# Kernel tuning notes

Hardware: AMD Instinct MI355X
Metric: run time of the kernel (lower is better)

Reference implementation:

```python
import jax, jax.numpy as jnp
import numpy as np

B, N, D_MODEL, H, DK, DV = 2, 2048, 512, 8, 64, 64


def setup_inputs() -> dict:
    key = jax.random.key(0)
    ks = jax.random.split(key, 15)
    s = 0.02
    f = jnp.float32
    inp = {
        "x": jax.random.normal(ks[0], (B, N, D_MODEL), f),
        # frozen base projections
        "Wq": jax.random.normal(ks[1], (D_MODEL, H * DK), f) * s,
        "bq": jax.random.normal(ks[2], (H * DK,), f) * s,
        "Wk": jax.random.normal(ks[3], (D_MODEL, H * DK), f) * s,
        "bk": jax.random.normal(ks[4], (H * DK,), f) * s,
        "Wv": jax.random.normal(ks[5], (D_MODEL, H * DV), f) * s,
        "bv": jax.random.normal(ks[6], (H * DV,), f) * s,
        # 'lora' adapters (full linears in the source, added to base)
        "Wq_lora": jax.random.normal(ks[7], (D_MODEL, H * DK), f) * s,
        "bq_lora": jax.random.normal(ks[8], (H * DK,), f) * s,
        "Wk_lora": jax.random.normal(ks[9], (D_MODEL, H * DK), f) * s,
        "bk_lora": jax.random.normal(ks[10], (H * DK,), f) * s,
        "Wv_lora": jax.random.normal(ks[11], (D_MODEL, H * DV), f) * s,
        "bv_lora": jax.random.normal(ks[12], (H * DV,), f) * s,
        # output projection
        "Wo": jax.random.normal(ks[13], (H * DV, D_MODEL), f) * s,
        "bo": jax.random.normal(ks[14], (D_MODEL,), f) * s,
    }
    return inp


def reference(x, Wq, bq, Wk, bk, Wv, bv,
              Wq_lora, bq_lora, Wk_lora, bk_lora, Wv_lora, bv_lora,
              Wo, bo):
    b, n, _ = x.shape
    # base + lora pairs share the same input -> fuse into single GEMMs
    q = x @ (Wq + Wq_lora) + (bq + bq_lora)          # [b, n, H*DK]
    k = x @ (Wk + Wk_lora) + (bk + bk_lora)          # [b, n, H*DK]
    v = x @ (Wv + Wv_lora) + (bv + bv_lora)          # [b, n, H*DV]

    q = q.reshape(b, n, H, DK).transpose(0, 2, 1, 3)  # [b, H, n, DK]
    k = k.reshape(b, n, H, DK).transpose(0, 2, 1, 3)
    v = v.reshape(b, n, H, DV).transpose(0, 2, 1, 3)

    scale = 1.0 / jnp.sqrt(jnp.asarray(DK, x.dtype))
    scores = jnp.einsum('bhqd,bhkd->bhqk', q, k) * scale  # [b, H, n, n]
    att = jax.nn.softmax(scores, axis=-1)                 # attn dropout = eval identity
    out = jnp.einsum('bhqk,bhkd->bhqd', att, v)           # [b, H, n, DV]
    out = out.transpose(0, 2, 1, 3).reshape(b, n, H * DV)
    return out @ Wo + bo                                  # resid dropout = eval identity
```

## Files before the change

kernel.cpp:

```cpp
#include <hip/hip_runtime.h>
#include <hip/hip_bf16.h>

#define B_  2
#define N_  2048
#define DM_ 512
#define H_  8
#define DK_ 64
#define DV_ 64
#define BN_ (B_*N_)
#define SPLITS 2

typedef __attribute__((ext_vector_type(8))) short short8;
typedef __attribute__((ext_vector_type(4))) float f32x4;
typedef unsigned short ushort;
typedef __attribute__((address_space(3))) unsigned int lds_u32_t;
typedef const __attribute__((address_space(1))) unsigned int glb_u32_t;

static __device__ __forceinline__ ushort f2bf(float x) {
    unsigned int u = __float_as_uint(x);
    unsigned int r = (u + 0x7FFFu + ((u >> 16) & 1u)) >> 16;
    return (ushort)r;
}
static __device__ __forceinline__ float bf2f(ushort u) {
    return __uint_as_float(((unsigned)u) << 16);
}
static __device__ __forceinline__ float exp2_fast(float x) {
    float r; asm("v_exp_f32 %0, %1" : "=v"(r) : "v"(x)); return r;
}
static __device__ __forceinline__ unsigned cvt_pk_bf16(float a, float b) {
    unsigned r; asm("v_cvt_pk_bf16_f32 %0, %1, %2" : "=v"(r) : "v"(a), "v"(b)); return r;
}

#define LOG2E 1.4426950408889634f

__global__ __launch_bounds__(256) void fuse_transpose4(
        const float* __restrict__ W0, const float* __restrict__ L0,
        const float* __restrict__ W1, const float* __restrict__ L1,
        const float* __restrict__ W2, const float* __restrict__ L2,
        const float* __restrict__ W3, ushort* __restrict__ WtBase) {
    const int z = blockIdx.z;
    const float* W  = (z == 0) ? W0 : (z == 1) ? W1 : (z == 2) ? W2 : W3;
    const float* WL = (z == 0) ? L0 : (z == 1) ? L1 : (z == 2) ? L2 : nullptr;
    ushort* Wt = WtBase + (size_t)z * DM_ * DM_;

    __shared__ float Ws[32][65];
    const int t  = threadIdx.x;
    const int c0 = blockIdx.x * 64;
    const int k0 = blockIdx.y * 32;
    {
        int r = t >> 4, cq = t & 15;
#pragma unroll
        for (int it = 0; it < 2; ++it) {
            int rr = r + it * 16;
            float4 v = *reinterpret_cast<const float4*>(W + (size_t)(k0 + rr) * DM_ + c0 + cq * 4);
            if (WL) {
                float4 u = *reinterpret_cast<const float4*>(WL + (size_t)(k0 + rr) * DM_ + c0 + cq * 4);
                v.x += u.x; v.y += u.y; v.z += u.z; v.w += u.w;
            }
            Ws[rr][cq * 4 + 0] = v.x; Ws[rr][cq * 4 + 1] = v.y;
            Ws[rr][cq * 4 + 2] = v.z; Ws[rr][cq * 4 + 3] = v.w;
        }
    }
    __syncthreads();
    {
        int cr = t >> 2, kq = t & 3;
        short8 o;
#pragma unroll
        for (int j = 0; j < 8; ++j) o[j] = (short)f2bf(Ws[kq * 8 + j][cr]);
        *reinterpret_cast<short8*>(Wt + (size_t)(c0 + cr) * DM_ + k0 + kq * 8) = o;
    }
}

__global__ void xcast_bias(const float* __restrict__ x, ushort* __restrict__ xb,
                           const float* __restrict__ bq, const float* __restrict__ bqL,
                           const float* __restrict__ bk, const float* __restrict__ bkL,
                           const float* __restrict__ bv, const float* __restrict__ bvL,
                           float* __restrict__ fb) {
    const int bid = blockIdx.x;
    if (bid < 1024) {
        size_t idx = (size_t)bid * blockDim.x + threadIdx.x;
        float4 v0 = *reinterpret_cast<const float4*>(x + idx * 8);
        float4 v1 = *reinterpret_cast<const float4*>(x + idx * 8 + 4);
        short8 o;
        o[0] = (short)f2bf(v0.x); o[1] = (short)f2bf(v0.y);
        o[2] = (short)f2bf(v0.z); o[3] = (short)f2bf(v0.w);
        o[4] = (short)f2bf(v1.x); o[5] = (short)f2bf(v1.y);
        o[6] = (short)f2bf(v1.z); o[7] = (short)f2bf(v1.w);
        *reinterpret_cast<short8*>(xb + idx * 8) = o;
    } else {
        int idx = (bid - 1024) * 256 + threadIdx.x;
        if (idx < 3 * DM_) {
            int w = idx >> 9, i = idx & 511;
            const float* a = (w == 0) ? bq : (w == 1) ? bk : bv;
            const float* b = (w == 0) ? bqL : (w == 1) ? bkL : bvL;
            fb[idx] = a[i] + b[i];
        }
    }
}

template<int BN, int MODE>
__global__ __launch_bounds__(256) void gemm_bf16(const ushort* __restrict__ A,
                                                 const ushort* __restrict__ Bt,
                                                 const float* __restrict__ bias,
                                                 ushort* __restrict__ Qd,
                                                 ushort* __restrict__ Kd,
                                                 ushort* __restrict__ Vd,
                                                 float* __restrict__ outF) {
    constexpr int NWC = BN / 64;
    constexpr int NWR = 4 / NWC;
    constexpr int MI  = (128 / NWR) / 16;
    constexpr int NJ  = 4;
    constexpr int BIT = BN / 32;
    const int rt = blockIdx.x, ct = blockIdx.y;
    __shared__ ushort As[2][128 * 64];
    __shared__ ushort Bs[2][BN * 64];
    const int t = threadIdx.x, lane = t & 63, w = t >> 6;
    const int wr = w / NWC, wc = w % NWC;
    const int lg = lane >> 4, lr = lane & 15;
    const int rowbase = wr * (128 / NWR);
    const int colbase = wc * 64;

    f32x4 acc[MI][NJ];
#pragma unroll
    for (int mi = 0; mi < MI; ++mi)
#pragma unroll
        for (int nj = 0; nj < NJ; ++nj) acc[mi][nj] = (f32x4){0.f, 0.f, 0.f, 0.f};

    auto stage = [&](int buf, int k0) {
#pragma unroll
        for (int it = 0; it < 4; ++it) {
            int c = it * 256 + t;
            int r = c >> 3, cq = c & 7;
            int gq = cq ^ (r & 7);
            __builtin_amdgcn_global_load_lds(
                (glb_u32_t*)(A + ((size_t)(rt * 128 + r)) * DM_ + k0 + gq * 8),
                (lds_u32_t*)((char*)(As[buf]) + c * 16), 16, 0, 0);
        }
#pragma unroll
        for (int it = 0; it < BIT; ++it) {
            int c = it * 256 + t;
            int r = c >> 3, cq = c & 7;
            int gq = cq ^ (r & 7);
            __builtin_amdgcn_global_load_lds(
                (glb_u32_t*)(Bt + ((size_t)(ct * BN + r)) * DM_ + k0 + gq * 8),
                (lds_u32_t*)((char*)(Bs[buf]) + c * 16), 16, 0, 0);
        }
    };

    stage(0, 0);
    __syncthreads();

    for (int k0 = 0; k0 < DM_; k0 += 64) {
        const int cur = (k0 >> 6) & 1;
        if (k0 + 64 < DM_) stage(cur ^ 1, k0 + 64);
#pragma unroll
        for (int kh = 0; kh < 2; ++kh) {
            short8 a[MI], b[NJ];
#pragma unroll
            for (int mi = 0; mi < MI; ++mi) {
                int row = rowbase + mi * 16 + lr;
                a[mi] = *reinterpret_cast<const short8*>(
                    (char*)(As[cur]) + row * 128 + (((kh * 4 + lg) ^ (row & 7)) << 4));
            }
#pragma unroll
            for (int nj = 0; nj < NJ; ++nj) {
                int row = colbase + nj * 16 + lr;
                b[nj] = *reinterpret_cast<const short8*>(
                    (char*)(Bs[cur]) + row * 128 + (((kh * 4 + lg) ^ (row & 7)) << 4));
            }
#pragma unroll
            for (int mi = 0; mi < MI; ++mi)
#pragma unroll
                for (int nj = 0; nj < NJ; ++nj)
                    acc[mi][nj] = __builtin_amdgcn_mfma_f32_16x16x32_bf16(
                        a[mi], b[nj], acc[mi][nj], 0, 0, 0);
        }
        __syncthreads();
    }

#pragma unroll
    for (int mi = 0; mi < MI; ++mi) {
#pragma unroll
        for (int nj = 0; nj < NJ; ++nj) {
#pragma unroll
            for (int r = 0; r < 4; ++r) {
                int m = rt * 128 + rowbase + mi * 16 + 4 * lg + r;
                int n = ct * BN + colbase + nj * 16 + lr;
                float v = acc[mi][nj][r] + bias[n];
                if (MODE == 0) {
                    int ws_ = n >> 9;
                    if (ws_ == 0) v *= 0.125f * LOG2E;
                    ushort* op = (ws_ == 0) ? Qd : (ws_ == 1) ? Kd : Vd;
                    int hd = (n >> 6) & 7, d = n & 63;
                    int bb = m >> 11, nn = m & (N_ - 1);
                    op[(((size_t)(bb * H_ + hd)) * N_ + nn) * DK_ + d] = f2bf(v);
                } else {
                    outF[(size_t)m * DM_ + n] = v;
                }
            }
        }
    }
}

__global__ __launch_bounds__(256) void vtrans(const ushort* __restrict__ Vd,
                                              ushort* __restrict__ Vt) {
    const int bh = blockIdx.y, nt = blockIdx.x;
    __shared__ ushort Ls[64 * 64];
    char* LB = (char*)Ls;
    const int t = threadIdx.x;
#pragma unroll
    for (int i = 0; i < 2; ++i) {
        int c = t + i * 256;
        int tok = c >> 3, dc = c & 7;
        uint4 v = *reinterpret_cast<const uint4*>(
            Vd + ((size_t)bh * N_ + nt * 64 + tok) * DV_ + dc * 8);
        int sw = dc ^ (tok & 7) ^ ((tok >> 3) & 7);
        *reinterpret_cast<uint4*>(LB + tok * 128 + (sw << 4)) = v;
    }
    __syncthreads();
#pragma unroll
    for (int i = 0; i < 2; ++i) {
        int c = t + i * 256;
        int d = c >> 3, tc = c & 7;
        short8 g;
#pragma unroll
        for (int j = 0; j < 8; ++j) {
            int tok = tc * 8 + j;
            int sw = (d >> 3) ^ (tok & 7) ^ ((tok >> 3) & 7);
            g[j] = *reinterpret_cast<const ushort*>(LB + tok * 128 + (sw << 4) + (d & 7) * 2);
        }
        *reinterpret_cast<short8*>(Vt + ((size_t)bh * DV_ + d) * N_ + nt * 64 + tc * 8) = g;
    }
}

__global__ __launch_bounds__(512) void attn_mfma(const ushort* __restrict__ Q,
                                                 const ushort* __restrict__ K,
                                                 const ushort* __restrict__ Vt,
                                                 ushort* __restrict__ Opart,
                                                 float2* __restrict__ Ml) {
    const int bh = blockIdx.y;
    const int qt = blockIdx.x;
    const int sp = blockIdx.z;
    const int t  = threadIdx.x;
    const int lane = t & 63;
    const int w  = t >> 6;
    const int lg = lane >> 4;
    const int lr = lane & 15;

    __shared__ ushort KsBuf[2][64 * 64];
    __shared__ ushort VtBuf[2][64 * 64];
    __shared__ ushort Ps[8][16 * 64];
    char* PsB = (char*)(Ps[w]);

    const ushort* Kb  = K  + ((size_t)bh * N_ + sp * (N_ / 2)) * DK_;
    const ushort* Vtb = Vt + (size_t)bh * DV_ * N_ + sp * (N_ / 2);

    const int srow = t >> 3, sc = t & 7;
    const int gsc = sc ^ (srow & 7);

    short8 qf[2];
    {
        const ushort* qrow = Q + ((size_t)bh * N_ + qt * 128 + w * 16 + lr) * DK_;
        qf[0] = *reinterpret_cast<const short8*>(qrow + 8 * lg);
        qf[1] = *reinterpret_cast<const short8*>(qrow + 32 + 8 * lg);
    }

    f32x4 o_[4];
#pragma unroll
    for (int i = 0; i < 4; i++) o_[i] = (f32x4){0.f, 0.f, 0.f, 0.f};
    float m1 = -1e30f, l1 = 0.f;

    auto stage = [&](int kt_, int buf_) {
        __builtin_amdgcn_global_load_lds(
            (glb_u32_t*)(Kb + ((size_t)(kt_ * 64 + srow)) * DK_ + gsc * 8),
            (lds_u32_t*)((char*)(KsBuf[buf_]) + t * 16), 16, 0, 0);
        __builtin_amdgcn_global_load_lds(
            (glb_u32_t*)(Vtb + (size_t)srow * N_ + kt_ * 64 + gsc * 8),
            (lds_u32_t*)((char*)(VtBuf[buf_]) + t * 16), 16, 0, 0);
    };

    stage(0, 0);
    __syncthreads();

    const int NT = (N_ / 2) / 64;
    for (int kt = 0; kt < NT; ++kt) {
        const int cur = kt & 1;
        if (kt + 1 < NT) stage(kt + 1, cur ^ 1);

        char* KsB = (char*)(KsBuf[cur]);
        char* VtB = (char*)(VtBuf[cur]);

        f32x4 s[4];
#pragma unroll
        for (int kb = 0; kb < 4; ++kb) {
            int row = kb * 16 + lr;
            short8 k0 = *reinterpret_cast<const short8*>(
                KsB + row * 128 + ((lg ^ (row & 7)) << 4));
            short8 k1 = *reinterpret_cast<const short8*>(
                KsB + row * 128 + (((4 + lg) ^ (row & 7)) << 4));
            f32x4 z = (f32x4){0.f, 0.f, 0.f, 0.f};
            s[kb] = __builtin_amdgcn_mfma_f32_16x16x32_bf16(k0, qf[0], z, 0, 0, 0);
            s[kb] = __builtin_amdgcn_mfma_f32_16x16x32_bf16(k1, qf[1], s[kb], 0, 0, 0);
        }

        float mx = s[0][0];
#pragma unroll
        for (int kb = 0; kb < 4; ++kb)
#pragma unroll
            for (int r = 0; r < 4; ++r) mx = fmaxf(mx, s[kb][r]);
        mx = fmaxf(mx, __shfl_xor(mx, 16));
        mx = fmaxf(mx, __shfl_xor(mx, 32));

        if (!__all(mx <= m1 + 8.0f)) {
            float mnew = fmaxf(m1, mx);
            float alpha = exp2_fast(m1 - mnew);
            m1 = mnew;
            l1 *= alpha;
#pragma unroll
            for (int r = 0; r < 4; ++r) {
                float ar = __shfl(alpha, 4 * lg + r);
#pragma unroll
                for (int db = 0; db < 4; ++db) o_[db][r] *= ar;
            }
        }

        float p[4][4];
        float sum = 0.f;
#pragma unroll
        for (int kb = 0; kb < 4; ++kb)
#pragma unroll
            for (int r = 0; r < 4; ++r) { p[kb][r] = exp2_fast(s[kb][r] - m1); sum += p[kb][r]; }
        sum += __shfl_xor(sum, 16);
        sum += __shfl_xor(sum, 32);
        l1 += sum;

#pragma unroll
        for (int kb = 0; kb < 4; ++kb) {
            uint2 pk;
            pk.x = cvt_pk_bf16(p[kb][0], p[kb][1]);
            pk.y = cvt_pk_bf16(p[kb][2], p[kb][3]);
            int chunk = 2 * kb + (lg >> 1);
            *reinterpret_cast<uint2*>(
                PsB + lr * 128 + ((chunk ^ (lr & 7)) << 4) + (lg & 1) * 8) = pk;
        }

        short8 pf[2];
        {
            pf[0] = *reinterpret_cast<const short8*>(
                PsB + lr * 128 + ((lg ^ (lr & 7)) << 4));
            pf[1] = *reinterpret_cast<const short8*>(
                PsB + lr * 128 + (((4 + lg) ^ (lr & 7)) << 4));
        }
#pragma unroll
        for (int db = 0; db < 4; ++db) {
            int row = db * 16 + lr;
            short8 v0 = *reinterpret_cast<const short8*>(
                VtB + row * 128 + ((lg ^ (row & 7)) << 4));
            short8 v1 = *reinterpret_cast<const short8*>(
                VtB + row * 128 + (((4 + lg) ^ (row & 7)) << 4));
            o_[db] = __builtin_amdgcn_mfma_f32_16x16x32_bf16(pf[0], v0, o_[db], 0, 0, 0);
            o_[db] = __builtin_amdgcn_mfma_f32_16x16x32_bf16(pf[1], v1, o_[db], 0, 0, 0);
        }

        __syncthreads();
    }

    const size_t rowbase = ((size_t)(sp * 16 + bh)) * N_ + qt * 128 + w * 16;
#pragma unroll
    for (int r = 0; r < 4; ++r) {
        int n_loc = 4 * lg + r;
#pragma unroll
        for (int db = 0; db < 4; ++db) {
            Opart[(rowbase + n_loc) * DV_ + db * 16 + lr] = f2bf(o_[db][r]);
        }
    }
    if (lg == 0) {
        Ml[rowbase + lr] = make_float2(m1, l1);
    }
}

__global__ __launch_bounds__(256) void merge_splits(const ushort* __restrict__ Opart,
                                                    const float2* __restrict__ Ml,
                                                    ushort* __restrict__ Od) {
    int gid = blockIdx.x * 256 + threadIdx.x;
    int row = gid >> 4;
    int dv  = (gid & 15) * 4;
    const int R = 16 * N_;
    float2 ml0 = Ml[row];
    float2 ml1 = Ml[R + row];
    float M  = fmaxf(ml0.x, ml1.x);
    float w0 = exp2_fast(ml0.x - M);
    float w1 = exp2_fast(ml1.x - M);
    float inv = 1.f / (w0 * ml0.y + w1 * ml1.y);
    uint2 a = *reinterpret_cast<const uint2*>(Opart + (size_t)row * DV_ + dv);
    uint2 b = *reinterpret_cast<const uint2*>(Opart + ((size_t)R + row) * DV_ + dv);
    const ushort* ae = reinterpret_cast<const ushort*>(&a);
    const ushort* be = reinterpret_cast<const ushort*>(&b);
    uint2 o;
    unsigned* oe = reinterpret_cast<unsigned*>(&o);
#pragma unroll
    for (int half = 0; half < 2; ++half) {
        float v0 = (w0 * bf2f(ae[half * 2 + 0]) + w1 * bf2f(be[half * 2 + 0])) * inv;
        float v1 = (w0 * bf2f(ae[half * 2 + 1]) + w1 * bf2f(be[half * 2 + 1])) * inv;
        oe[half] = cvt_pk_bf16(v0, v1);
    }
    int bh = row >> 11, n = row & (N_ - 1);
    int bb = bh >> 3, h = bh & 7;
    *reinterpret_cast<uint2*>(Od + ((size_t)(bb * N_ + n)) * (H_ * DV_) + h * DV_ + dv) = o;
}

extern "C" void kernel_launch(void* const* d_in, const int* in_sizes, int n_in,
                              void* d_out, int out_size, void* d_ws, size_t ws_size,
                              hipStream_t stream) {
    const float* x   = (const float*)d_in[0];
    const float* Wq  = (const float*)d_in[1];
    const float* bq  = (const float*)d_in[2];
    const float* Wk  = (const float*)d_in[3];
    const float* bk  = (const float*)d_in[4];
    const float* Wv  = (const float*)d_in[5];
    const float* bv  = (const float*)d_in[6];
    const float* WqL = (const float*)d_in[7];
    const float* bqL = (const float*)d_in[8];
    const float* WkL = (const float*)d_in[9];
    const float* bkL = (const float*)d_in[10];
    const float* WvL = (const float*)d_in[11];
    const float* bvL = (const float*)d_in[12];
    const float* Wo  = (const float*)d_in[13];
    const float* bo  = (const float*)d_in[14];

    ushort* Wt_all = (ushort*)d_ws;
    ushort* Wot    = Wt_all + (size_t)3 * DM_ * DM_;
    float*  fb     = (float*)(Wt_all + (size_t)4 * DM_ * DM_);
    ushort* xbf    = (ushort*)(fb + 3 * DM_);
    ushort* Qd     = xbf + (size_t)BN_ * DM_;
    ushort* Kd     = Qd + (size_t)B_ * H_ * N_ * DK_;
    ushort* Vd     = Kd + (size_t)B_ * H_ * N_ * DK_;
    ushort* Vtd    = Vd + (size_t)B_ * H_ * N_ * DV_;
    ushort* Od     = Vtd + (size_t)B_ * H_ * N_ * DV_;
    ushort* Opart  = Od + (size_t)B_ * H_ * N_ * DV_;
    float2* Ml     = (float2*)(Opart + (size_t)SPLITS * B_ * H_ * N_ * DV_);

    float* out = (float*)d_out;

    fuse_transpose4<<<dim3(8, 16, 4), 256, 0, stream>>>(Wq, WqL, Wk, WkL, Wv, WvL, Wo, Wt_all);
    xcast_bias<<<1030, 256, 0, stream>>>(x, xbf, bq, bqL, bk, bkL, bv, bvL, fb);

    gemm_bf16<128, 0><<<dim3(32, 12), 256, 0, stream>>>(xbf, Wt_all, fb, Qd, Kd, Vd, nullptr);
    vtrans<<<dim3(32, 16), 256, 0, stream>>>(Vd, Vtd);
    attn_mfma<<<dim3(16, 16, SPLITS), 512, 0, stream>>>(Qd, Kd, Vtd, Opart, Ml);
    merge_splits<<<(B_ * H_ * N_ * 16) / 256, 256, 0, stream>>>(Opart, Ml, Od);
    gemm_bf16<64, 1><<<dim3(32, 8), 256, 0, stream>>>(Od, Wot, bo, nullptr, nullptr, nullptr, out);
}
```

Before: 78.22 us.

## Merge prep kernels and stage attention K/V tiles through registers

Folds the weight fuse-transpose and the x cast/bias-sum kernels into a single launch, removing one kernel launch and its dispatch gap. In the attention kernel, direct global-to-LDS async loads are replaced with register-staged prefetch: the next K/V tile is loaded into registers at the top of the iteration and written to the swizzled LDS buffer after the PV MFMAs. This lets the global load latency overlap compute, at the cost of extra VGPRs and explicit LDS write instructions.

```diff
diff --git a/kernel.cpp b/kernel.cpp
--- a/kernel.cpp
+++ b/kernel.cpp
@@ -33,52 +33,49 @@
 
 #define LOG2E 1.4426950408889634f
 
-__global__ __launch_bounds__(256) void fuse_transpose4(
+__global__ __launch_bounds__(256) void prep(
         const float* __restrict__ W0, const float* __restrict__ L0,
         const float* __restrict__ W1, const float* __restrict__ L1,
         const float* __restrict__ W2, const float* __restrict__ L2,
-        const float* __restrict__ W3, ushort* __restrict__ WtBase) {
-    const int z = blockIdx.z;
-    const float* W  = (z == 0) ? W0 : (z == 1) ? W1 : (z == 2) ? W2 : W3;
-    const float* WL = (z == 0) ? L0 : (z == 1) ? L1 : (z == 2) ? L2 : nullptr;
-    ushort* Wt = WtBase + (size_t)z * DM_ * DM_;
-
-    __shared__ float Ws[32][65];
-    const int t  = threadIdx.x;
-    const int c0 = blockIdx.x * 64;
-    const int k0 = blockIdx.y * 32;
-    {
-        int r = t >> 4, cq = t & 15;
-#pragma unroll
-        for (int it = 0; it < 2; ++it) {
-            int rr = r + it * 16;
-            float4 v = *reinterpret_cast<const float4*>(W + (size_t)(k0 + rr) * DM_ + c0 + cq * 4);
-            if (WL) {
-                float4 u = *reinterpret_cast<const float4*>(WL + (size_t)(k0 + rr) * DM_ + c0 + cq * 4);
-                v.x += u.x; v.y += u.y; v.z += u.z; v.w += u.w;
+        const float* __restrict__ W3, ushort* __restrict__ WtBase,
+        const float* __restrict__ x, ushort* __restrict__ xb,
+        const float* __restrict__ bq, const float* __restrict__ bqL,
+        const float* __restrict__ bk, const float* __restrict__ bkL,
+        const float* __restrict__ bv, const float* __restrict__ bvL,
+        float* __restrict__ fb) {
+    const int bid = blockIdx.x;
+    const int t = threadIdx.x;
+    if (bid < 512) {
+        const int z = bid >> 7, rem = bid & 127;
+        const int c0 = (rem & 7) * 64, k0 = (rem >> 3) * 32;
+        const float* W  = (z == 0) ? W0 : (z == 1) ? W1 : (z == 2) ? W2 : W3;
+        const float* WL = (z == 0) ? L0 : (z == 1) ? L1 : (z == 2) ? L2 : nullptr;
+        ushort* Wt = WtBase + (size_t)z * DM_ * DM_;
+        __shared__ float Ws[32][65];
+        {
+            int r = t >> 4, cq = t & 15;
+#pragma unroll
+            for (int it = 0; it < 2; ++it) {
+                int rr = r + it * 16;
+                float4 v = *reinterpret_cast<const float4*>(W + (size_t)(k0 + rr) * DM_ + c0 + cq * 4);
+                if (WL) {
+                    float4 u = *reinterpret_cast<const float4*>(WL + (size_t)(k0 + rr) * DM_ + c0 + cq * 4);
+                    v.x += u.x; v.y += u.y; v.z += u.z; v.w += u.w;
+                }
+                Ws[rr][cq * 4 + 0] = v.x; Ws[rr][cq * 4 + 1] = v.y;
+                Ws[rr][cq * 4 + 2] = v.z; Ws[rr][cq * 4 + 3] = v.w;
             }
-            Ws[rr][cq * 4 + 0] = v.x; Ws[rr][cq * 4 + 1] = v.y;
-            Ws[rr][cq * 4 + 2] = v.z; Ws[rr][cq * 4 + 3] = v.w;
-        }
-    }
-    __syncthreads();
-    {
-        int cr = t >> 2, kq = t & 3;
-        short8 o;
-#pragma unroll
-        for (int j = 0; j < 8; ++j) o[j] = (short)f2bf(Ws[kq * 8 + j][cr]);
-        *reinterpret_cast<short8*>(Wt + (size_t)(c0 + cr) * DM_ + k0 + kq * 8) = o;
-    }
-}
-
-__global__ void xcast_bias(const float* __restrict__ x, ushort* __restrict__ xb,
-                           const float* __restrict__ bq, const float* __restrict__ bqL,
-                           const float* __restrict__ bk, const float* __restrict__ bkL,
-                           const float* __restrict__ bv, const float* __restrict__ bvL,
-                           float* __restrict__ fb) {
-    const int bid = blockIdx.x;
-    if (bid < 1024) {
-        size_t idx = (size_t)bid * blockDim.x + threadIdx.x;
+        }
+        __syncthreads();
+        {
+            int cr = t >> 2, kq = t & 3;
+            short8 o;
+#pragma unroll
+            for (int j = 0; j < 8; ++j) o[j] = (short)f2bf(Ws[kq * 8 + j][cr]);
+            *reinterpret_cast<short8*>(Wt + (size_t)(c0 + cr) * DM_ + k0 + kq * 8) = o;
+        }
+    } else if (bid < 1536) {
+        size_t idx = (size_t)(bid - 512) * 256 + t;
         float4 v0 = *reinterpret_cast<const float4*>(x + idx * 8);
         float4 v1 = *reinterpret_cast<const float4*>(x + idx * 8 + 4);
         short8 o;
@@ -88,7 +85,7 @@
         o[6] = (short)f2bf(v1.z); o[7] = (short)f2bf(v1.w);
         *reinterpret_cast<short8*>(xb + idx * 8) = o;
     } else {
-        int idx = (bid - 1024) * 256 + threadIdx.x;
+        int idx = (bid - 1536) * 256 + t;
         if (idx < 3 * DM_) {
             int w = idx >> 9, i = idx & 511;
             const float* a = (w == 0) ? bq : (w == 1) ? bk : bv;
@@ -256,7 +253,6 @@
     const ushort* Vtb = Vt + (size_t)bh * DV_ * N_ + sp * (N_ / 2);
 
     const int srow = t >> 3, sc = t & 7;
-    const int gsc = sc ^ (srow & 7);
 
     short8 qf[2];
     {
@@ -270,22 +266,24 @@
     for (int i = 0; i < 4; i++) o_[i] = (f32x4){0.f, 0.f, 0.f, 0.f};
     float m1 = -1e30f, l1 = 0.f;
 
-    auto stage = [&](int kt_, int buf_) {
-        __builtin_amdgcn_global_load_lds(
-            (glb_u32_t*)(Kb + ((size_t)(kt_ * 64 + srow)) * DK_ + gsc * 8),
-            (lds_u32_t*)((char*)(KsBuf[buf_]) + t * 16), 16, 0, 0);
-        __builtin_amdgcn_global_load_lds(
-            (glb_u32_t*)(Vtb + (size_t)srow * N_ + kt_ * 64 + gsc * 8),
-            (lds_u32_t*)((char*)(VtBuf[buf_]) + t * 16), 16, 0, 0);
+    uint4 kreg, vreg;
+    auto issue = [&](int kt_) {
+        kreg = *reinterpret_cast<const uint4*>(Kb  + ((size_t)(kt_ * 64 + srow)) * DK_ + sc * 8);
+        vreg = *reinterpret_cast<const uint4*>(Vtb + (size_t)srow * N_ + kt_ * 64 + sc * 8);
     };
-
-    stage(0, 0);
+    auto wstage = [&](int buf_) {
+        *reinterpret_cast<uint4*>((char*)(KsBuf[buf_]) + srow * 128 + ((sc ^ (srow & 7)) << 4)) = kreg;
+        *reinterpret_cast<uint4*>((char*)(VtBuf[buf_]) + srow * 128 + ((sc ^ (srow & 7)) << 4)) = vreg;
+    };
+
+    issue(0);
+    wstage(0);
     __syncthreads();
 
     const int NT = (N_ / 2) / 64;
     for (int kt = 0; kt < NT; ++kt) {
         const int cur = kt & 1;
-        if (kt + 1 < NT) stage(kt + 1, cur ^ 1);
+        if (kt + 1 < NT) issue(kt + 1);
 
         char* KsB = (char*)(KsBuf[cur]);
         char* VtB = (char*)(VtBuf[cur]);
@@ -362,6 +360,7 @@
             o_[db] = __builtin_amdgcn_mfma_f32_16x16x32_bf16(pf[1], v1, o_[db], 0, 0, 0);
         }
 
+        if (kt + 1 < NT) wstage(cur ^ 1);
         __syncthreads();
     }
 
@@ -442,8 +441,8 @@
 
     float* out = (float*)d_out;
 
-    fuse_transpose4<<<dim3(8, 16, 4), 256, 0, stream>>>(Wq, WqL, Wk, WkL, Wv, WvL, Wo, Wt_all);
-    xcast_bias<<<1030, 256, 0, stream>>>(x, xbf, bq, bqL, bk, bkL, bv, bvL, fb);
+    prep<<<1542, 256, 0, stream>>>(Wq, WqL, Wk, WkL, Wv, WvL, Wo, Wt_all,
+                                   x, xbf, bq, bqL, bk, bkL, bv, bvL, fb);
 
     gemm_bf16<128, 0><<<dim3(32, 12), 256, 0, stream>>>(xbf, Wt_all, fb, Qd, Kd, Vd, nullptr);
     vtrans<<<dim3(32, 16), 256, 0, stream>>>(Vd, Vtd);
```

Result: faster. 72.28 us (-7.6%).
